# Kernel optimization log

Hardware: AMD Instinct MI355X
Metric: run time of the kernel (lower is better)

## Reference

```python
import jax, jax.numpy as jnp
import numpy as np

B, N, C, H = 16, 207, 64, 64

def setup_inputs() -> dict:
    key = jax.random.key(0)
    k1, k2, k3, k4, k5 = jax.random.split(key, 5)
    return {
        "x": jax.random.normal(k1, (B, N, C), dtype=jnp.float32),
        "state": jax.random.normal(k2, (B, N, 1, H), dtype=jnp.float32),
        "Wx": jax.random.normal(k3, (B, N, C, 3 * H), dtype=jnp.float32) * 0.1,
        "Wh": jax.random.normal(k4, (B, N, H, 3 * H), dtype=jnp.float32) * 0.1,
        "b": jax.random.normal(k5, (B, N, 1, 3 * H), dtype=jnp.float32) * 0.1,
    }

def reference(x, state, Wx, Wh, b):
    # x: [B,N,C] -> [B,N,1,C]; state (h): [B,N,1,H]
    if x.ndim == 3:
        x = x[..., None, :]
    h = state
    dim_hidden = Wh.shape[-2]
    # One fused batched matmul for x @ Wx, then split into r/z/c parts.
    xW = jnp.matmul(x, Wx)  # [B,N,1,3H]
    xr, xz, xc = jnp.split(xW, 3, axis=-1)
    Wrh, Wzh, Wch = jnp.split(Wh, 3, axis=-1)
    br, bz, bc = jnp.split(b, 3, axis=-1)
    r = jax.nn.sigmoid(xr + jnp.matmul(h, Wrh) + br)
    z = jax.nn.sigmoid(xz + jnp.matmul(h, Wzh) + bz)
    # Note torch precedence: r * h @ Wch == (r * h) @ Wch
    hc = jnp.tanh(xc + jnp.matmul(r * h, Wch) + bc)
    h_new = (1.0 - z) * h + z * hc  # [B,N,1,H]
    return h_new
```

## Files before the change

kernel.cpp:

```cpp
#include <hip/hip_runtime.h>
#include <math.h>


#define GC 64
#define GH 64
#define J3 192

__global__ __launch_bounds__(192) void gru_cell_kernel(
    const float* __restrict__ x,
    const float* __restrict__ state,
    const float* __restrict__ Wx,
    const float* __restrict__ Wh,
    const float* __restrict__ b,
    float* __restrict__ out)
{
    const int pos = blockIdx.x;
    const int j = threadIdx.x;

    __shared__ float x_s[GC];
    __shared__ float h_s[GH];
    __shared__ float wch_s[GC][GH];
    __shared__ float rh_s[GH];
    __shared__ float z_s[GH];

    const size_t wbase = (size_t)pos * GC * J3;
    const float* Wxp = Wx + wbase;
    const float* Whp = Wh + wbase;

    if (j < GC)           x_s[j]      = x[(size_t)pos * GC + j];
    else if (j < GC + GH) h_s[j - GC] = state[(size_t)pos * GH + (j - GC)];
    __syncthreads();

    float accx = 0.f, acch = 0.f;
    const bool is_c = (j >= 128);
    const int jc = j - 128;
    #pragma unroll 8
    for (int c = 0; c < GC; ++c) {
        float wx = Wxp[c * J3 + j];
        float wh = Whp[c * J3 + j];
        accx += x_s[c] * wx;
        acch += h_s[c] * wh;
        if (is_c) wch_s[c][jc] = wh;
    }

    const float bj = b[(size_t)pos * J3 + j];
    const float t = accx + bj;

    if (j < GH) {
        float r = 1.f / (1.f + expf(-(t + acch)));
        rh_s[j] = r * h_s[j];
    } else if (j < 2 * GH) {
        float z = 1.f / (1.f + expf(-(t + acch)));
        z_s[j - GH] = z;
    }
    __syncthreads();

    if (is_c) {
        float s = 0.f;
        #pragma unroll 8
        for (int k = 0; k < GH; ++k) s += rh_s[k] * wch_s[k][jc];
        float hc = tanhf(t + s);
        float z = z_s[jc];
        out[(size_t)pos * GH + jc] = (1.f - z) * h_s[jc] + z * hc;
    }
}

extern "C" void kernel_launch(void* const* d_in, const int* in_sizes, int n_in,
                              void* d_out, int out_size, void* d_ws, size_t ws_size,
                              hipStream_t stream) {
    const float* x     = (const float*)d_in[0];
    const float* state = (const float*)d_in[1];
    const float* Wx    = (const float*)d_in[2];
    const float* Wh    = (const float*)d_in[3];
    const float* b     = (const float*)d_in[4];
    float* out = (float*)d_out;

    const int npos = in_sizes[0] / GC;

    gru_cell_kernel<<<npos, 192, 0, stream>>>(x, state, Wx, Wh, b, out);
}
```

Before: 366.5 us.

## Vectorize weight loads to float4 and split reduction across thread groups

Each thread now loads float4 weight chunks, covering 4 output columns over a quarter of the input rows, and partial sums are reduced through shared memory. This replaces scalar 4-byte loads with 16-byte loads, issuing fewer, wider memory transactions on a heavily bandwidth-bound kernel. It adds a shared-memory partial-sum buffer and an extra barrier. The staging of the candidate-gate weights into shared memory is also done with float4 stores.

```diff
diff --git a/kernel.cpp b/kernel.cpp
--- a/kernel.cpp
+++ b/kernel.cpp
@@ -5,8 +5,9 @@
 #define GC 64
 #define GH 64
 #define J3 192
+#define WPP (GC * J3)
 
-__global__ __launch_bounds__(192) void gru_cell_kernel(
+__global__ __launch_bounds__(192) void gru_cell_v2(
     const float* __restrict__ x,
     const float* __restrict__ state,
     const float* __restrict__ Wx,
@@ -15,52 +16,66 @@
     float* __restrict__ out)
 {
     const int pos = blockIdx.x;
-    const int j = threadIdx.x;
+    const int t = threadIdx.x;
+    const int jg = t % 48;
+    const int rp = t / 48;
 
     __shared__ float x_s[GC];
     __shared__ float h_s[GH];
-    __shared__ float wch_s[GC][GH];
+    __shared__ float wch_s[GC * GH];
+    __shared__ float part[4][J3 + 4];
     __shared__ float rh_s[GH];
     __shared__ float z_s[GH];
 
-    const size_t wbase = (size_t)pos * GC * J3;
-    const float* Wxp = Wx + wbase;
-    const float* Whp = Wh + wbase;
-
-    if (j < GC)           x_s[j]      = x[(size_t)pos * GC + j];
-    else if (j < GC + GH) h_s[j - GC] = state[(size_t)pos * GH + (j - GC)];
+    if (t < GC)           x_s[t]      = x[(size_t)pos * GC + t];
+    else if (t < GC + GH) h_s[t - GC] = state[(size_t)pos * GH + (t - GC)];
     __syncthreads();
 
-    float accx = 0.f, acch = 0.f;
-    const bool is_c = (j >= 128);
-    const int jc = j - 128;
-    #pragma unroll 8
-    for (int c = 0; c < GC; ++c) {
-        float wx = Wxp[c * J3 + j];
-        float wh = Whp[c * J3 + j];
-        accx += x_s[c] * wx;
-        acch += h_s[c] * wh;
-        if (is_c) wch_s[c][jc] = wh;
+    const float4* __restrict__ Wx4 = (const float4*)(Wx + (size_t)pos * WPP);
+    const float4* __restrict__ Wh4 = (const float4*)(Wh + (size_t)pos * WPP);
+
+    float4 acc = {0.f, 0.f, 0.f, 0.f};
+    const bool gate = (jg < 32);
+    const int wchcol = 4 * (jg - 32);
+
+    #pragma unroll 4
+    for (int i = 0; i < 16; ++i) {
+        const int c = 4 * i + rp;
+        float4 wx4 = Wx4[i * J3 + t];
+        float4 wh4 = Wh4[i * J3 + t];
+        const float xs = x_s[c];
+        acc.x += xs * wx4.x; acc.y += xs * wx4.y;
+        acc.z += xs * wx4.z; acc.w += xs * wx4.w;
+        if (gate) {
+            const float hs = h_s[c];
+            acc.x += hs * wh4.x; acc.y += hs * wh4.y;
+            acc.z += hs * wh4.z; acc.w += hs * wh4.w;
+        } else {
+            *((float4*)&wch_s[c * GH + wchcol]) = wh4;
+        }
     }
 
-    const float bj = b[(size_t)pos * J3 + j];
-    const float t = accx + bj;
+    *((float4*)&part[rp][4 * jg]) = acc;
+    __syncthreads();
 
-    if (j < GH) {
-        float r = 1.f / (1.f + expf(-(t + acch)));
-        rh_s[j] = r * h_s[j];
-    } else if (j < 2 * GH) {
-        float z = 1.f / (1.f + expf(-(t + acch)));
-        z_s[j - GH] = z;
+    float v = part[0][t] + part[1][t] + part[2][t] + part[3][t]
+            + b[(size_t)pos * J3 + t];
+    const float tc = v;
+    if (t < GH) {
+        float r = 1.f / (1.f + expf(-v));
+        rh_s[t] = r * h_s[t];
+    } else if (t < 2 * GH) {
+        z_s[t - GH] = 1.f / (1.f + expf(-v));
     }
     __syncthreads();
 
-    if (is_c) {
+    if (t >= 2 * GH) {
+        const int jc = t - 2 * GH;
         float s = 0.f;
         #pragma unroll 8
-        for (int k = 0; k < GH; ++k) s += rh_s[k] * wch_s[k][jc];
-        float hc = tanhf(t + s);
-        float z = z_s[jc];
+        for (int k = 0; k < GH; ++k) s += rh_s[k] * wch_s[k * GH + jc];
+        const float hc = tanhf(tc + s);
+        const float z = z_s[jc];
         out[(size_t)pos * GH + jc] = (1.f - z) * h_s[jc] + z * hc;
     }
 }
@@ -77,5 +92,5 @@
 
     const int npos = in_sizes[0] / GC;
 
-    gru_cell_kernel<<<npos, 192, 0, stream>>>(x, state, Wx, Wh, b, out);
+    gru_cell_v2<<<npos, 192, 0, stream>>>(x, state, Wx, Wh, b, out);
 }
```

After: 338.2 us. 1.08x faster.

## Use one wavefront per position with shuffle broadcasts instead of shared memory

Applied to the files above, without the earlier changes.

Each position is now handled by a single 64-lane wavefront where every lane computes the r, z and candidate gates for one hidden unit. Inputs are broadcast with warp shuffles instead of shared memory, which removes all barriers and the shared staging of the candidate weight block. The candidate weights are re-read from global memory after the gates are computed. This trades extra global/L2 traffic for more loads in flight per thread and no block synchronisation.

```diff
diff --git a/kernel.cpp b/kernel.cpp
--- a/kernel.cpp
+++ b/kernel.cpp
@@ -5,8 +5,9 @@
 #define GC 64
 #define GH 64
 #define J3 192
+#define WPP (GC * J3)
 
-__global__ __launch_bounds__(192) void gru_cell_kernel(
+__global__ __launch_bounds__(64, 4) void gru_cell_v5(
     const float* __restrict__ x,
     const float* __restrict__ state,
     const float* __restrict__ Wx,
@@ -17,52 +18,59 @@
     const int pos = blockIdx.x;
     const int j = threadIdx.x;
 
-    __shared__ float x_s[GC];
-    __shared__ float h_s[GH];
-    __shared__ float wch_s[GC][GH];
-    __shared__ float rh_s[GH];
-    __shared__ float z_s[GH];
+    const float xj = x[(size_t)pos * GC + j];
+    const float hj = state[(size_t)pos * GH + j];
 
-    const size_t wbase = (size_t)pos * GC * J3;
-    const float* Wxp = Wx + wbase;
-    const float* Whp = Wh + wbase;
+    const float* __restrict__ Wxp = Wx + (size_t)pos * WPP + j;
+    const float* __restrict__ Whp = Wh + (size_t)pos * WPP + j;
 
-    if (j < GC)           x_s[j]      = x[(size_t)pos * GC + j];
-    else if (j < GC + GH) h_s[j - GC] = state[(size_t)pos * GH + (j - GC)];
-    __syncthreads();
+    float axr = 0.f, axz = 0.f, axc = 0.f, ahr = 0.f, ahz = 0.f;
 
-    float accx = 0.f, acch = 0.f;
-    const bool is_c = (j >= 128);
-    const int jc = j - 128;
-    #pragma unroll 8
-    for (int c = 0; c < GC; ++c) {
-        float wx = Wxp[c * J3 + j];
-        float wh = Whp[c * J3 + j];
-        accx += x_s[c] * wx;
-        acch += h_s[c] * wh;
-        if (is_c) wch_s[c][jc] = wh;
+    #pragma unroll 2
+    for (int c0 = 0; c0 < GC; c0 += 4) {
+        float wxr[4], wxz[4], wxc[4], whr[4], whz[4];
+        #pragma unroll
+        for (int u = 0; u < 4; ++u) {
+            const float* px = Wxp + (size_t)(c0 + u) * J3;
+            wxr[u] = px[0];
+            wxz[u] = px[64];
+            wxc[u] = px[128];
+            const float* ph = Whp + (size_t)(c0 + u) * J3;
+            whr[u] = ph[0];
+            whz[u] = ph[64];
+        }
+        #pragma unroll
+        for (int u = 0; u < 4; ++u) {
+            const float xs = __shfl(xj, c0 + u, 64);
+            const float hs = __shfl(hj, c0 + u, 64);
+            axr += xs * wxr[u];
+            axz += xs * wxz[u];
+            axc += xs * wxc[u];
+            ahr += hs * whr[u];
+            ahz += hs * whz[u];
+        }
     }
 
-    const float bj = b[(size_t)pos * J3 + j];
-    const float t = accx + bj;
+    const float* __restrict__ bp = b + (size_t)pos * J3 + j;
+    const float br = bp[0], bz = bp[64], bc = bp[128];
 
-    if (j < GH) {
-        float r = 1.f / (1.f + expf(-(t + acch)));
-        rh_s[j] = r * h_s[j];
-    } else if (j < 2 * GH) {
-        float z = 1.f / (1.f + expf(-(t + acch)));
-        z_s[j - GH] = z;
+    const float r = 1.f / (1.f + expf(-(axr + ahr + br)));
+    const float z = 1.f / (1.f + expf(-(axz + ahz + bz)));
+    const float rh = r * hj;
+
+    const float* __restrict__ Wch = Wh + (size_t)pos * WPP + 2 * GH + j;
+    float s = 0.f;
+    #pragma unroll 2
+    for (int c0 = 0; c0 < GC; c0 += 8) {
+        float w[8];
+        #pragma unroll
+        for (int u = 0; u < 8; ++u) w[u] = Wch[(size_t)(c0 + u) * J3];
+        #pragma unroll
+        for (int u = 0; u < 8; ++u) s += __shfl(rh, c0 + u, 64) * w[u];
     }
-    __syncthreads();
 
-    if (is_c) {
-        float s = 0.f;
-        #pragma unroll 8
-        for (int k = 0; k < GH; ++k) s += rh_s[k] * wch_s[k][jc];
-        float hc = tanhf(t + s);
-        float z = z_s[jc];
-        out[(size_t)pos * GH + jc] = (1.f - z) * h_s[jc] + z * hc;
-    }
+    const float hc = tanhf(axc + s + bc);
+    out[(size_t)pos * GH + j] = (1.f - z) * hj + z * hc;
 }
 
 extern "C" void kernel_launch(void* const* d_in, const int* in_sizes, int n_in,
@@ -77,5 +85,5 @@
 
     const int npos = in_sizes[0] / GC;
 
-    gru_cell_kernel<<<npos, 192, 0, stream>>>(x, state, Wx, Wh, b, out);
+    gru_cell_v5<<<npos, 64, 0, stream>>>(x, state, Wx, Wh, b, out);
 }
```

New measurement: 340.2 us. 1.08x faster.
